# Optimization experiments

Measured on AMD Instinct MI355X. Metric: run time of the kernel, lower is better.

## Reference

```python
import jax, jax.numpy as jnp
import numpy as np

PIXEL_W = 1.0
EPS = 1e-8
BIG = 1e10


def extract_zero_crossings(s):
    """Vectorized marching-squares-style zero-crossing extraction.
    s: (H, W) SDF. Returns padded points (N, 2) float and validity mask (N,) bool,
    N = (H-1)*W + H*(W-1), in the same (vertical pairs first, then horizontal)
    order as the original python loops."""
    H, W = s.shape
    dt = s.dtype
    # vertical neighbor pairs (i, j) vs (i+1, j)
    v1, v2 = s[:-1, :], s[1:, :]
    ii = jnp.broadcast_to(jnp.arange(H - 1, dtype=dt)[:, None], (H - 1, W))
    jj = jnp.broadcast_to(jnp.arange(W, dtype=dt)[None, :], (H - 1, W))
    c1 = v1 == 0
    c2 = (~c1) & (v2 == 0)
    cx = (~c1) & (~c2) & (v1 * v2 < 0)
    alpha = jnp.abs(v1) / (jnp.abs(v1) + jnp.abs(v2) + EPS)
    row = jnp.where(c1, ii, jnp.where(c2, ii + 1.0, ii + alpha))
    pts_v = jnp.stack([row, jj], axis=-1).reshape(-1, 2)
    m_v = (c1 | c2 | cx).reshape(-1)
    # horizontal neighbor pairs (i, j) vs (i, j+1)
    h1, h2 = s[:, :-1], s[:, 1:]
    ii2 = jnp.broadcast_to(jnp.arange(H, dtype=dt)[:, None], (H, W - 1))
    jj2 = jnp.broadcast_to(jnp.arange(W - 1, dtype=dt)[None, :], (H, W - 1))
    d1 = h1 == 0
    d2 = (~d1) & (h2 == 0)
    dx = (~d1) & (~d2) & (h1 * h2 < 0)
    beta = jnp.abs(h1) / (jnp.abs(h1) + jnp.abs(h2) + EPS)
    col = jnp.where(d1, jj2, jnp.where(d2, jj2 + 1.0, jj2 + beta))
    pts_h = jnp.stack([ii2, col], axis=-1).reshape(-1, 2)
    m_h = (d1 | d2 | dx).reshape(-1)
    return jnp.concatenate([pts_v, pts_h], 0), jnp.concatenate([m_v, m_h], 0)


def pairwise_dist(p, g):
    # (Np, Ng) euclidean distances via the gram trick (avoids (Np,Ng,2) temp)
    d2 = jnp.sum(p * p, 1)[:, None] + jnp.sum(g * g, 1)[None, :] - 2.0 * (p @ g.T)
    return jnp.sqrt(jnp.maximum(d2, 0.0))


def masked_chamfer(pp, pm, gp, gm):
    # chamfer as in compute_chamfer_distance: -mean(min over gt) + mean(min over pred)
    d = pairwise_dist(pp, gp)
    d = jnp.where(pm[:, None] & gm[None, :], d, BIG)
    min_p = jnp.min(d, axis=1)
    min_g = jnp.min(d, axis=0)
    np_ = jnp.maximum(jnp.sum(pm), 1)
    ng_ = jnp.maximum(jnp.sum(gm), 1)
    return -jnp.sum(jnp.where(pm, min_p, 0.0)) / np_ + jnp.sum(jnp.where(gm, min_g, 0.0)) / ng_


def setup_inputs() -> dict:
    key = jax.random.key(0)
    k1, k2 = jax.random.split(key)
    B, H, W = 2, 80, 80
    return {
        "pred_logits": jax.random.normal(k1, (B, 1, H, W), dtype=jnp.float32),
        "gt_sdf": jax.random.normal(k2, (B, 1, H, W), dtype=jnp.float32),
    }


def reference(pred_logits, gt_sdf):
    pred = pred_logits[:, 0]  # (B, H, W)
    gt = gt_sdf[:, 0]
    pixel_loss = jnp.mean(jnp.abs(pred - gt))
    chamfers = []
    for b in range(pred.shape[0]):  # small fixed batch loop
        pp, pm = extract_zero_crossings(pred[b])
        gp, gm = extract_zero_crossings(gt[b])
        chamfers.append(masked_chamfer(pp, pm, gp, gm))
    loss = PIXEL_W * pixel_loss
    last_chamfer = jnp.mean(jnp.stack(chamfers))
    return loss, last_chamfer
```

## Files before the change

kernel.cpp:

```cpp
#include <hip/hip_runtime.h>

#define HH 80
#define WW 80
#define IMG (HH * WW)
#define NV ((HH - 1) * WW)
#define NPTS (NV + HH * (WW - 1))
#define NPIX (2 * IMG)
#define BIGF 1.0e10f
#define INVC 1.0e7f
#define EPSF 1e-8f
#define QSCALE 131072.0f

#define SETPAD 12800
#define SBLOCKS (SETPAD / 256)
#define EXBLOCKS (4 * SBLOCKS)
#define PXBLOCKS (NPIX / 256)
#define PREPB (EXBLOCKS + PXBLOCKS)

#define BLK 256
#define APT 8
#define ACHUNK (BLK * APT)
#define ABLOCKS ((NPTS + ACHUNK - 1) / ACHUNK)
#define NSLICE 32
#define MAXSLICE ((((NPTS + NSLICE - 1) / NSLICE) + 1) & ~1)
#define MAXP2 (MAXSLICE / 2)

#define CNT_STRIDE 32
#define PIX_OFF 512
#define TICKET_OFF 640
#define SUM_OFF 768
#define SCALAR_BYTES 1024

typedef float f32x2 __attribute__((ext_vector_type(2)));

__device__ __forceinline__ long long wave_reduce_ll(long long v) {
#pragma unroll
  for (int o = 32; o > 0; o >>= 1) {
    int2 p = *(int2*)&v;
    p.x = __shfl_down(p.x, o, 64);
    p.y = __shfl_down(p.y, o, 64);
    v += *(long long*)&p;
  }
  return v;
}

__global__ void k_zero(unsigned int* __restrict__ w) {
  w[threadIdx.x] = 0u;
}

__global__ void __launch_bounds__(256) k_prep(
    const float* __restrict__ pred, const float* __restrict__ gt,
    float2* __restrict__ pts, float* __restrict__ minarr,
    int* __restrict__ cnt, unsigned long long* __restrict__ pix_i) {
  __shared__ int wc[4], wo[4];
  __shared__ long long rl[4];
  int tid = threadIdx.x, lane = tid & 63, wid = tid >> 6;
  int gtid = blockIdx.x * 256 + tid;

  if (gtid < 4 * NPTS) minarr[gtid] = BIGF;

  if (blockIdx.x < EXBLOCKS) {
    int set = blockIdx.x / SBLOCKS;
    int idx = (blockIdx.x % SBLOCKS) * 256 + tid;
    const float* s = (set < 2 ? pred : gt) + (set & 1) * IMG;
    float r = 0.f, c = 0.f;
    bool valid = false;
    if (idx < NPTS) {
      if (idx < NV) {
        int i = idx / WW, j = idx - i * WW;
        float v1 = s[i * WW + j], v2 = s[(i + 1) * WW + j];
        c = (float)j;
        if (v1 == 0.f)      { r = (float)i;       valid = true; }
        else if (v2 == 0.f) { r = (float)i + 1.f; valid = true; }
        else {
          r = (float)i + fabsf(v1) / (fabsf(v1) + fabsf(v2) + EPSF);
          valid = (v1 * v2 < 0.f);
        }
      } else {
        int t = idx - NV;
        int i = t / (WW - 1), j = t - i * (WW - 1);
        float h1 = s[i * WW + j], h2 = s[i * WW + j + 1];
        r = (float)i;
        if (h1 == 0.f)      { c = (float)j;       valid = true; }
        else if (h2 == 0.f) { c = (float)j + 1.f; valid = true; }
        else {
          c = (float)j + fabsf(h1) / (fabsf(h1) + fabsf(h2) + EPSF);
          valid = (h1 * h2 < 0.f);
        }
      }
    }
    unsigned long long mask = __ballot(valid);
    int nw = __popcll(mask);
    if (lane == 0) wc[wid] = nw;
    __syncthreads();
    if (tid == 0) {
      int t0 = wc[0], t1 = wc[1], t2 = wc[2], t3 = wc[3];
      int tot = t0 + t1 + t2 + t3;
      int base = tot ? atomicAdd(&cnt[set * CNT_STRIDE], tot) : 0;
      wo[0] = base; wo[1] = base + t0; wo[2] = base + t0 + t1;
      wo[3] = base + t0 + t1 + t2;
    }
    __syncthreads();
    if (valid) {
      int lpos = __popcll(mask & ((1ull << lane) - 1ull));
      pts[set * NPTS + wo[wid] + lpos] = make_float2(r, c);
    }
  } else {
    int p = (blockIdx.x - EXBLOCKS) * 256 + tid;
    float d = fabsf(pred[p] - gt[p]);
    long long q = (long long)(d * QSCALE + 0.5f);
    q = wave_reduce_ll(q);
    if (lane == 0) rl[wid] = q;
    __syncthreads();
    if (tid == 0)
      atomicAdd(pix_i, (unsigned long long)(rl[0] + rl[1] + rl[2] + rl[3]));
  }
}

__global__ void __launch_bounds__(BLK) k_min(
    const float2* __restrict__ pts, float* __restrict__ minarr,
    const int* __restrict__ cnt) {
  int dir = blockIdx.z;
  int Aset = ((dir & 1) << 1) | (dir >> 1);
  int Bset = Aset ^ 2;
  int cntA = cnt[Aset * CNT_STRIDE], cntB = cnt[Bset * CNT_STRIDE];

  int abase0 = blockIdx.x * ACHUNK;
  if (abase0 >= cntA) return;
  int slicelen = (((cntB + NSLICE - 1) / NSLICE) + 1) & ~1;
  int b0 = blockIdx.y * slicelen;
  if (b0 >= cntB) return;
  int n = min(slicelen, cntB - b0);
  int sn = (n + 1) & ~1;

  __shared__ f32x2 qx_s[MAXP2], qy_s[MAXP2], q2_s[MAXP2];
  for (int i = threadIdx.x; i < sn; i += BLK) {
    float2 q = (i < n) ? pts[Bset * NPTS + b0 + i] : make_float2(INVC, INVC);
    ((float*)qx_s)[i] = q.x;
    ((float*)qy_s)[i] = q.y;
    ((float*)q2_s)[i] = fmaf(q.x, q.x, q.y * q.y);
  }
  __syncthreads();

  int abase = abase0 + threadIdx.x;
  f32x2 nxv[APT], nyv[APT];
  float p2v[APT], m[APT];
#pragma unroll
  for (int i = 0; i < APT; ++i) {
    int a = abase + i * BLK;
    float2 p = (a < cntA) ? pts[Aset * NPTS + a] : make_float2(0.f, 0.f);
    float nx = -2.f * p.x, ny = -2.f * p.y;
    nxv[i].x = nx; nxv[i].y = nx;
    nyv[i].x = ny; nyv[i].y = ny;
    p2v[i] = fmaf(p.x, p.x, p.y * p.y);
    m[i] = 3.0e38f;
  }

  int np2 = sn >> 1;
#pragma unroll 2
  for (int p = 0; p < np2; ++p) {
    f32x2 qx = qx_s[p], qy = qy_s[p], q2 = q2_s[p];
#pragma unroll
    for (int i = 0; i < APT; ++i) {
      f32x2 u = __builtin_elementwise_fma(
          nyv[i], qy, __builtin_elementwise_fma(nxv[i], qx, q2));
      m[i] = fminf(fminf(u.x, u.y), m[i]);
    }
  }

#pragma unroll
  for (int i = 0; i < APT; ++i) {
    int a = abase + i * BLK;
    if (a < cntA) {
      float d2 = fmaxf(m[i] + p2v[i], 0.f);
      unsigned int mine = __float_as_uint(d2);
      unsigned int* addr = (unsigned int*)&minarr[Aset * NPTS + a];
      unsigned int cur = __hip_atomic_load(addr, __ATOMIC_RELAXED,
                                           __HIP_MEMORY_SCOPE_AGENT);
      if (mine < cur) atomicMin(addr, mine);
    }
  }
}

__global__ void __launch_bounds__(256) k_fin(
    const float* __restrict__ minarr, const int* __restrict__ cnt,
    const unsigned long long* __restrict__ pix_i,
    unsigned long long* __restrict__ sum_i,
    unsigned int* __restrict__ ticket, float* __restrict__ out) {
  int set = blockIdx.x >> 2, q = blockIdx.x & 3;
  int tid = threadIdx.x, lane = tid & 63;
  int n = cnt[set * CNT_STRIDE];

  long long ls = 0;
  for (int i = q * 256 + tid; i < n; i += 1024) {
    float d = sqrtf(minarr[set * NPTS + i]);
    ls += (long long)(d * QSCALE + 0.5f);
  }
  ls = wave_reduce_ll(ls);
  if (lane == 0) atomicAdd(&sum_i[set], (unsigned long long)ls);
  __syncthreads();

  if (tid == 0) {
    __threadfence();
    unsigned int t = atomicAdd(ticket, 1u);
    if (t == 15u) {
      const float iq = 1.0f / QSCALE;
      float ss[4];
      for (int k = 0; k < 4; ++k)
        ss[k] = (float)((long long)atomicAdd(&sum_i[k], 0ull)) * iq;
      float n0 = fmaxf((float)cnt[0 * CNT_STRIDE], 1.f);
      float n1 = fmaxf((float)cnt[1 * CNT_STRIDE], 1.f);
      float n2 = fmaxf((float)cnt[2 * CNT_STRIDE], 1.f);
      float n3 = fmaxf((float)cnt[3 * CNT_STRIDE], 1.f);
      float ch0 = -ss[0] / n0 + ss[2] / n2;
      float ch1 = -ss[1] / n1 + ss[3] / n3;
      out[0] = (float)(long long)(*pix_i) * iq / (float)NPIX;
      out[1] = 0.5f * (ch0 + ch1);
    }
  }
}

extern "C" void kernel_launch(void* const* d_in, const int* in_sizes, int n_in,
                              void* d_out, int out_size, void* d_ws, size_t ws_size,
                              hipStream_t stream) {
  const float* pred = (const float*)d_in[0];
  const float* gt   = (const float*)d_in[1];
  float* out = (float*)d_out;

  int* cnt = (int*)d_ws;
  unsigned long long* pix_i = (unsigned long long*)((char*)d_ws + PIX_OFF);
  unsigned int* ticket = (unsigned int*)((char*)d_ws + TICKET_OFF);
  unsigned long long* sum_i = (unsigned long long*)((char*)d_ws + SUM_OFF);
  float2* pts   = (float2*)((char*)d_ws + SCALAR_BYTES);
  float* minarr = (float*)((char*)d_ws + SCALAR_BYTES + sizeof(float2) * 4 * NPTS);

  k_zero<<<1, 256, 0, stream>>>((unsigned int*)d_ws);
  k_prep<<<PREPB, 256, 0, stream>>>(pred, gt, pts, minarr, cnt, pix_i);
  k_min<<<dim3(ABLOCKS, NSLICE, 4), BLK, 0, stream>>>(pts, minarr, cnt);
  k_fin<<<16, 256, 0, stream>>>(minarr, cnt, pix_i, sum_i, ticket, out);
}
```

Measured before the change: 39.41 us.

## Precompute point norms in prep, read B points directly, widen final reduction

k_prep now stores each zero-crossing as a float4 (r, c, r²+c², 0), so the squared norm is computed once instead of in k_min. k_min drops its LDS staging and __syncthreads and reads B points straight from global memory, relying on uniform broadcast loads and cache hits, with a scalar tail for odd slice lengths. k_fin doubles its block count to 32 and issues fixed, unrolled loads so more minimum values are in flight at once. The risks are doubled point storage, and global-memory latency in the inner loop replacing LDS reads.

```diff
diff --git a/kernel.cpp b/kernel.cpp
--- a/kernel.cpp
+++ b/kernel.cpp
@@ -22,8 +22,9 @@
 #define ACHUNK (BLK * APT)
 #define ABLOCKS ((NPTS + ACHUNK - 1) / ACHUNK)
 #define NSLICE 32
-#define MAXSLICE ((((NPTS + NSLICE - 1) / NSLICE) + 1) & ~1)
-#define MAXP2 (MAXSLICE / 2)
+
+#define FINB 32
+#define FTRIPS 7
 
 #define CNT_STRIDE 32
 #define PIX_OFF 512
@@ -50,7 +51,7 @@
 
 __global__ void __launch_bounds__(256) k_prep(
     const float* __restrict__ pred, const float* __restrict__ gt,
-    float2* __restrict__ pts, float* __restrict__ minarr,
+    float4* __restrict__ pts, float* __restrict__ minarr,
     int* __restrict__ cnt, unsigned long long* __restrict__ pix_i) {
   __shared__ int wc[4], wo[4];
   __shared__ long long rl[4];
@@ -103,7 +104,8 @@
     __syncthreads();
     if (valid) {
       int lpos = __popcll(mask & ((1ull << lane) - 1ull));
-      pts[set * NPTS + wo[wid] + lpos] = make_float2(r, c);
+      pts[set * NPTS + wo[wid] + lpos] =
+          make_float4(r, c, fmaf(r, r, c * c), 0.f);
     }
   } else {
     int p = (blockIdx.x - EXBLOCKS) * 256 + tid;
@@ -118,7 +120,7 @@
 }
 
 __global__ void __launch_bounds__(BLK) k_min(
-    const float2* __restrict__ pts, float* __restrict__ minarr,
+    const float4* __restrict__ pts, float* __restrict__ minarr,
     const int* __restrict__ cnt) {
   int dir = blockIdx.z;
   int Aset = ((dir & 1) << 1) | (dir >> 1);
@@ -131,16 +133,6 @@
   int b0 = blockIdx.y * slicelen;
   if (b0 >= cntB) return;
   int n = min(slicelen, cntB - b0);
-  int sn = (n + 1) & ~1;
-
-  __shared__ f32x2 qx_s[MAXP2], qy_s[MAXP2], q2_s[MAXP2];
-  for (int i = threadIdx.x; i < sn; i += BLK) {
-    float2 q = (i < n) ? pts[Bset * NPTS + b0 + i] : make_float2(INVC, INVC);
-    ((float*)qx_s)[i] = q.x;
-    ((float*)qy_s)[i] = q.y;
-    ((float*)q2_s)[i] = fmaf(q.x, q.x, q.y * q.y);
-  }
-  __syncthreads();
 
   int abase = abase0 + threadIdx.x;
   f32x2 nxv[APT], nyv[APT];
@@ -148,23 +140,38 @@
 #pragma unroll
   for (int i = 0; i < APT; ++i) {
     int a = abase + i * BLK;
-    float2 p = (a < cntA) ? pts[Aset * NPTS + a] : make_float2(0.f, 0.f);
+    float4 p = (a < cntA) ? pts[Aset * NPTS + a]
+                          : make_float4(0.f, 0.f, 0.f, 0.f);
     float nx = -2.f * p.x, ny = -2.f * p.y;
     nxv[i].x = nx; nxv[i].y = nx;
     nyv[i].x = ny; nyv[i].y = ny;
-    p2v[i] = fmaf(p.x, p.x, p.y * p.y);
+    p2v[i] = p.z;
     m[i] = 3.0e38f;
   }
 
-  int np2 = sn >> 1;
+  const float4* __restrict__ bp = pts + Bset * NPTS + b0;
+  int np2 = n >> 1;
 #pragma unroll 2
   for (int p = 0; p < np2; ++p) {
-    f32x2 qx = qx_s[p], qy = qy_s[p], q2 = q2_s[p];
+    float4 b0v = bp[2 * p];
+    float4 b1v = bp[2 * p + 1];
+    f32x2 qx, qy, q2;
+    qx.x = b0v.x; qx.y = b1v.x;
+    qy.x = b0v.y; qy.y = b1v.y;
+    q2.x = b0v.z; q2.y = b1v.z;
 #pragma unroll
     for (int i = 0; i < APT; ++i) {
       f32x2 u = __builtin_elementwise_fma(
           nyv[i], qy, __builtin_elementwise_fma(nxv[i], qx, q2));
       m[i] = fminf(fminf(u.x, u.y), m[i]);
+    }
+  }
+  if (n & 1) {
+    float4 bl = bp[n - 1];
+#pragma unroll
+    for (int i = 0; i < APT; ++i) {
+      float t = fmaf(nyv[i].x, bl.y, fmaf(nxv[i].x, bl.x, bl.z));
+      m[i] = fminf(t, m[i]);
     }
   }
 
@@ -187,14 +194,21 @@
     const unsigned long long* __restrict__ pix_i,
     unsigned long long* __restrict__ sum_i,
     unsigned int* __restrict__ ticket, float* __restrict__ out) {
-  int set = blockIdx.x >> 2, q = blockIdx.x & 3;
+  int set = blockIdx.x >> 3, q = blockIdx.x & 7;
   int tid = threadIdx.x, lane = tid & 63;
   int n = cnt[set * CNT_STRIDE];
-
+  const float* base = minarr + set * NPTS;
+
+  float v[FTRIPS];
+#pragma unroll
+  for (int k = 0; k < FTRIPS; ++k) {
+    int a = q * 256 + tid + k * 2048;
+    v[k] = (a < n) ? base[a] : -1.f;
+  }
   long long ls = 0;
-  for (int i = q * 256 + tid; i < n; i += 1024) {
-    float d = sqrtf(minarr[set * NPTS + i]);
-    ls += (long long)(d * QSCALE + 0.5f);
+#pragma unroll
+  for (int k = 0; k < FTRIPS; ++k) {
+    if (v[k] >= 0.f) ls += (long long)(sqrtf(v[k]) * QSCALE + 0.5f);
   }
   ls = wave_reduce_ll(ls);
   if (lane == 0) atomicAdd(&sum_i[set], (unsigned long long)ls);
@@ -203,7 +217,7 @@
   if (tid == 0) {
     __threadfence();
     unsigned int t = atomicAdd(ticket, 1u);
-    if (t == 15u) {
+    if (t == FINB - 1) {
       const float iq = 1.0f / QSCALE;
       float ss[4];
       for (int k = 0; k < 4; ++k)
@@ -231,11 +245,11 @@
   unsigned long long* pix_i = (unsigned long long*)((char*)d_ws + PIX_OFF);
   unsigned int* ticket = (unsigned int*)((char*)d_ws + TICKET_OFF);
   unsigned long long* sum_i = (unsigned long long*)((char*)d_ws + SUM_OFF);
-  float2* pts   = (float2*)((char*)d_ws + SCALAR_BYTES);
-  float* minarr = (float*)((char*)d_ws + SCALAR_BYTES + sizeof(float2) * 4 * NPTS);
+  float4* pts   = (float4*)((char*)d_ws + SCALAR_BYTES);
+  float* minarr = (float*)((char*)d_ws + SCALAR_BYTES + sizeof(float4) * 4 * NPTS);
 
   k_zero<<<1, 256, 0, stream>>>((unsigned int*)d_ws);
   k_prep<<<PREPB, 256, 0, stream>>>(pred, gt, pts, minarr, cnt, pix_i);
   k_min<<<dim3(ABLOCKS, NSLICE, 4), BLK, 0, stream>>>(pts, minarr, cnt);
-  k_fin<<<16, 256, 0, stream>>>(minarr, cnt, pix_i, sum_i, ticket, out);
-}
+  k_fin<<<FINB, 256, 0, stream>>>(minarr, cnt, pix_i, sum_i, ticket, out);
+}
```

Result: slower. 44.48 us (+12.9%).
